# Performance work log

Measured on AMD Instinct MI355X. Metric: run time of the kernel, lower is better.

Reference implementation:

```python
import jax, jax.numpy as jnp
import numpy as np

ALPHA = 0.2

def _ema_last_weights(T, alpha, dtype):
    # Closed form for the final EMA value after the sequential recurrence:
    # ema_T = (1-a)^(T-1) * x_0 + sum_{t=1}^{T-1} a*(1-a)^(T-1-t) * x_t
    t = jnp.arange(T)
    w = alpha * (1.0 - alpha) ** (T - 1 - t)
    w = w.at[0].set((1.0 - alpha) ** (T - 1))
    return w.astype(dtype)


def setup_inputs() -> dict:
    key = jax.random.key(0)
    k1, k2 = jax.random.split(key)
    B, T, F = 64, 2048, 256
    x = jax.random.normal(k1, (B, T, F), dtype=jnp.float32)
    W = jax.random.normal(k2, (F, F), dtype=jnp.float32) * (1.0 / np.sqrt(F))
    b = jnp.zeros((F,), dtype=jnp.float32)
    return {"x": x, "W": W, "b": b}


def reference(x, W, b):
    B, T, F = x.shape
    # final-step EMA over time (equivalent to the sequential python loop)
    w = _ema_last_weights(T, ALPHA, x.dtype)          # [T]
    last_ref = jnp.einsum('t,btf->bf', w, x)[:, None, :]  # [B,1,F]
    # base residual predictor: per-timestep linear
    res = jnp.einsum('btf,fg->btg', x, W) + b          # [B,T,F]
    return last_ref + res
```

## Files before the change

kernel.cpp:

```cpp
#include <hip/hip_runtime.h>
#include <hip/hip_bf16.h>

#define Bdim 64
#define Tdim 2048
#define Fdim 256
#define TAIL 256
#define NCH 8
#define CHT 32

#define BM 64
#define BK 64
#define ASTR 72
#define BSTR 72

typedef __bf16 bf16x8 __attribute__((ext_vector_type(8)));
typedef float f32x16 __attribute__((ext_vector_type(16)));
typedef unsigned short u16x8 __attribute__((ext_vector_type(8)));

__device__ __forceinline__ unsigned short bf16_rne(float f) {
  unsigned int u = __float_as_uint(f);
  u += 0x7FFFu + ((u >> 16) & 1u);
  return (unsigned short)(u >> 16);
}

__global__ void prep_wt(const float* __restrict__ W, unsigned short* __restrict__ Wt) {
  int i = blockIdx.x * 256 + threadIdx.x;
  int g = i >> 8, f = i & 255;
  Wt[i] = bf16_rne(W[f * Fdim + g]);
}

__global__ void ema_partial(const float* __restrict__ x, float* __restrict__ part) {
  int b = blockIdx.x, c = blockIdx.y, f = threadIdx.x;
  int t0 = Tdim - TAIL + c * CHT;
  float w = 0.2f * exp2f((float)(Tdim - 1 - t0) * -0.32192809488736235f);
  const float* xp = x + ((size_t)b * Tdim + t0) * Fdim + f;
  float s = 0.f;
#pragma unroll
  for (int j = 0; j < CHT; ++j) {
    s += w * xp[(size_t)j * Fdim];
    w *= 1.25f;
  }
  part[(c * Bdim + b) * Fdim + f] = s;
}

__global__ __launch_bounds__(256, 3)
void gemm_fused(const float* __restrict__ x, const unsigned short* __restrict__ Wt,
                const float* __restrict__ bias, const float* __restrict__ part,
                float* __restrict__ out) {
  __shared__ unsigned short Abuf[BM * ASTR];
  __shared__ unsigned short Bbuf[Fdim * BSTR];
  __shared__ float lref[Fdim];

  const int tid = threadIdx.x;
  const int blk = blockIdx.x;
  const int b = blk >> 5;
  const size_t row0 = (size_t)blk * BM;

  {
    float s = bias[tid];
#pragma unroll
    for (int c = 0; c < NCH; ++c) s += part[(c * Bdim + b) * Fdim + tid];
    lref[tid] = s;
  }

  const int wave = tid >> 6;
  const int lane = tid & 63;
  const int lm = lane & 31;
  const int half = lane >> 5;

  f32x16 acc[2][2] = {};

  const int g8 = (tid & 7) * 8;
  const int arow = tid >> 3;

  for (int kc = 0; kc < 4; ++kc) {
    const int k0 = kc * BK;
#pragma unroll
    for (int p = 0; p < 2; ++p) {
      int r = arow + p * 32;
      const float* src = &x[(row0 + r) * Fdim + k0 + g8];
      float4 v0 = *(const float4*)src;
      float4 v1 = *(const float4*)(src + 4);
      u16x8 w;
      w[0] = bf16_rne(v0.x); w[1] = bf16_rne(v0.y);
      w[2] = bf16_rne(v0.z); w[3] = bf16_rne(v0.w);
      w[4] = bf16_rne(v1.x); w[5] = bf16_rne(v1.y);
      w[6] = bf16_rne(v1.z); w[7] = bf16_rne(v1.w);
      *(u16x8*)&Abuf[r * ASTR + g8] = w;
    }
#pragma unroll
    for (int p = 0; p < 8; ++p) {
      int n = arow + p * 32;
      u16x8 wv = *(const u16x8*)&Wt[n * Fdim + k0 + g8];
      *(u16x8*)&Bbuf[n * BSTR + g8] = wv;
    }
    __syncthreads();

    const int ko = half * 8;
#pragma unroll
    for (int s = 0; s < 4; ++s) {
      int kk = s * 16 + ko;
      bf16x8 a0 = *(const bf16x8*)&Abuf[(lm) * ASTR + kk];
      bf16x8 a1 = *(const bf16x8*)&Abuf[(32 + lm) * ASTR + kk];
      bf16x8 b0 = *(const bf16x8*)&Bbuf[(wave * 64 + lm) * BSTR + kk];
      bf16x8 b1 = *(const bf16x8*)&Bbuf[(wave * 64 + 32 + lm) * BSTR + kk];
      acc[0][0] = __builtin_amdgcn_mfma_f32_32x32x16_bf16(a0, b0, acc[0][0], 0, 0, 0);
      acc[0][1] = __builtin_amdgcn_mfma_f32_32x32x16_bf16(a0, b1, acc[0][1], 0, 0, 0);
      acc[1][0] = __builtin_amdgcn_mfma_f32_32x32x16_bf16(a1, b0, acc[1][0], 0, 0, 0);
      acc[1][1] = __builtin_amdgcn_mfma_f32_32x32x16_bf16(a1, b1, acc[1][1], 0, 0, 0);
    }
    __syncthreads();
  }

  float* op = out + row0 * Fdim;
  const int rbase = 4 * half;
#pragma unroll
  for (int i = 0; i < 2; ++i) {
#pragma unroll
    for (int j = 0; j < 2; ++j) {
      int n = wave * 64 + j * 32 + lm;
      float lb = lref[n];
#pragma unroll
      for (int r = 0; r < 16; ++r) {
        int rowi = i * 32 + (r & 3) + 8 * (r >> 2) + rbase;
        op[(size_t)rowi * Fdim + n] = acc[i][j][r] + lb;
      }
    }
  }
}

extern "C" void kernel_launch(void* const* d_in, const int* in_sizes, int n_in,
                              void* d_out, int out_size, void* d_ws, size_t ws_size,
                              hipStream_t stream) {
  const float* x = (const float*)d_in[0];
  const float* W = (const float*)d_in[1];
  const float* bias = (const float*)d_in[2];
  float* out = (float*)d_out;

  unsigned short* Wt = (unsigned short*)d_ws;
  float* part = (float*)((char*)d_ws + Fdim * Fdim * sizeof(unsigned short));

  prep_wt<<<Fdim, 256, 0, stream>>>(W, Wt);
  ema_partial<<<dim3(Bdim, NCH), 256, 0, stream>>>(x, part);
  gemm_fused<<<(Bdim * Tdim) / BM, 256, 0, stream>>>(x, Wt, bias, part, out);
}
```

Before: 242.3 us.

## Double-buffer GEMM LDS tiles with register prefetch, XOR swizzle, and merged prep kernels

Restructures the GEMM main loop into 8 chunks of K=32, with double-buffered LDS tiles. Global loads for the next chunks are prefetched into registers while MFMAs run on the current buffer. Padded LDS strides are replaced by an XOR swizzle, and only one barrier per chunk is needed. The W transpose and the EMA partial kernels are merged into one launch to cut a kernel launch. This costs more registers for the prefetch state, which may pressure occupancy at 3 blocks per CU.

```diff
diff --git a/kernel.cpp b/kernel.cpp
--- a/kernel.cpp
+++ b/kernel.cpp
@@ -1,5 +1,4 @@
 #include <hip/hip_runtime.h>
-#include <hip/hip_bf16.h>
 
 #define Bdim 64
 #define Tdim 2048
@@ -9,9 +8,8 @@
 #define CHT 32
 
 #define BM 64
-#define BK 64
-#define ASTR 72
-#define BSTR 72
+#define BK 32
+#define NCHUNK 8
 
 typedef __bf16 bf16x8 __attribute__((ext_vector_type(8)));
 typedef float f32x16 __attribute__((ext_vector_type(16)));
@@ -23,38 +21,47 @@
   return (unsigned short)(u >> 16);
 }
 
-__global__ void prep_wt(const float* __restrict__ W, unsigned short* __restrict__ Wt) {
-  int i = blockIdx.x * 256 + threadIdx.x;
-  int g = i >> 8, f = i & 255;
-  Wt[i] = bf16_rne(W[f * Fdim + g]);
-}
-
-__global__ void ema_partial(const float* __restrict__ x, float* __restrict__ part) {
-  int b = blockIdx.x, c = blockIdx.y, f = threadIdx.x;
-  int t0 = Tdim - TAIL + c * CHT;
-  float w = 0.2f * exp2f((float)(Tdim - 1 - t0) * -0.32192809488736235f);
-  const float* xp = x + ((size_t)b * Tdim + t0) * Fdim + f;
-  float s = 0.f;
+__global__ void prep(const float* __restrict__ x, const float* __restrict__ W,
+                     unsigned short* __restrict__ Wt, float* __restrict__ part) {
+  int blk = blockIdx.x;
+  if (blk < Fdim) {
+    int i = blk * 256 + threadIdx.x;
+    int g = i >> 8, f = i & 255;
+    Wt[i] = bf16_rne(W[f * Fdim + g]);
+  } else {
+    int j = blk - Fdim;
+    int b = j & 63, c = j >> 6;
+    int f = threadIdx.x;
+    int t0 = Tdim - TAIL + c * CHT;
+    float w = 0.2f * exp2f((float)(Tdim - 1 - t0) * -0.32192809488736235f);
+    const float* xp = x + ((size_t)b * Tdim + t0) * Fdim + f;
+    float s = 0.f;
 #pragma unroll
-  for (int j = 0; j < CHT; ++j) {
-    s += w * xp[(size_t)j * Fdim];
-    w *= 1.25f;
+    for (int q = 0; q < CHT; ++q) {
+      s += w * xp[(size_t)q * Fdim];
+      w *= 1.25f;
+    }
+    part[(c * Bdim + b) * Fdim + f] = s;
   }
-  part[(c * Bdim + b) * Fdim + f] = s;
 }
 
 __global__ __launch_bounds__(256, 3)
 void gemm_fused(const float* __restrict__ x, const unsigned short* __restrict__ Wt,
                 const float* __restrict__ bias, const float* __restrict__ part,
                 float* __restrict__ out) {
-  __shared__ unsigned short Abuf[BM * ASTR];
-  __shared__ unsigned short Bbuf[Fdim * BSTR];
+  __shared__ unsigned short Abuf[2][BM * BK];
+  __shared__ unsigned short Bbuf[2][Fdim * BK];
   __shared__ float lref[Fdim];
 
   const int tid = threadIdx.x;
   const int blk = blockIdx.x;
   const int b = blk >> 5;
   const size_t row0 = (size_t)blk * BM;
+
+  const int wave = tid >> 6;
+  const int lane = tid & 63;
+  const int lm = lane & 31;
+  const int half = lane >> 5;
 
   {
     float s = bias[tid];
@@ -63,53 +70,85 @@
     lref[tid] = s;
   }
 
-  const int wave = tid >> 6;
-  const int lane = tid & 63;
-  const int lm = lane & 31;
-  const int half = lane >> 5;
+  const int ar = tid >> 2;
+  const int ag = tid & 3;
+  const int aoff = ar * BK + ((ag ^ (ar & 3)) << 3);
+  const float* asrc = x + (row0 + ar) * Fdim + ag * 8;
+
+  const int bn = tid >> 2;
+  const int bg = tid & 3;
+  const unsigned short* bsrc = Wt + (size_t)bn * Fdim + bg * 8;
+  const int boff = bn * BK + ((bg ^ (bn & 3)) << 3);
 
   f32x16 acc[2][2] = {};
+  float4 Ar[2][2];
+  u16x8 br0, br1, br2, br3;
 
-  const int g8 = (tid & 7) * 8;
-  const int arow = tid >> 3;
+  Ar[0][0] = *(const float4*)(asrc);
+  Ar[0][1] = *(const float4*)(asrc + 4);
+  br0 = *(const u16x8*)(bsrc + 0 * 64 * Fdim);
+  br1 = *(const u16x8*)(bsrc + 1 * 64 * Fdim);
+  br2 = *(const u16x8*)(bsrc + 2 * 64 * Fdim);
+  br3 = *(const u16x8*)(bsrc + 3 * 64 * Fdim);
+  {
+    float4 v0 = Ar[0][0], v1 = Ar[0][1];
+    u16x8 w;
+    w[0] = bf16_rne(v0.x); w[1] = bf16_rne(v0.y);
+    w[2] = bf16_rne(v0.z); w[3] = bf16_rne(v0.w);
+    w[4] = bf16_rne(v1.x); w[5] = bf16_rne(v1.y);
+    w[6] = bf16_rne(v1.z); w[7] = bf16_rne(v1.w);
+    *(u16x8*)&Abuf[0][aoff] = w;
+  }
+  *(u16x8*)&Bbuf[0][boff + 0 * 64 * BK] = br0;
+  *(u16x8*)&Bbuf[0][boff + 1 * 64 * BK] = br1;
+  *(u16x8*)&Bbuf[0][boff + 2 * 64 * BK] = br2;
+  *(u16x8*)&Bbuf[0][boff + 3 * 64 * BK] = br3;
+  Ar[1][0] = *(const float4*)(asrc + BK);
+  Ar[1][1] = *(const float4*)(asrc + BK + 4);
+  __syncthreads();
 
-  for (int kc = 0; kc < 4; ++kc) {
-    const int k0 = kc * BK;
 #pragma unroll
-    for (int p = 0; p < 2; ++p) {
-      int r = arow + p * 32;
-      const float* src = &x[(row0 + r) * Fdim + k0 + g8];
-      float4 v0 = *(const float4*)src;
-      float4 v1 = *(const float4*)(src + 4);
+  for (int c = 0; c < NCHUNK; ++c) {
+    const int cur = c & 1, nxt = cur ^ 1;
+    if (c + 2 < NCHUNK) {
+      const float* s4 = asrc + (c + 2) * BK;
+      Ar[cur][0] = *(const float4*)(s4);
+      Ar[cur][1] = *(const float4*)(s4 + 4);
+    }
+    if (c + 1 < NCHUNK) {
+      const unsigned short* bs = bsrc + (c + 1) * BK;
+      br0 = *(const u16x8*)(bs + 0 * 64 * Fdim);
+      br1 = *(const u16x8*)(bs + 1 * 64 * Fdim);
+      br2 = *(const u16x8*)(bs + 2 * 64 * Fdim);
+      br3 = *(const u16x8*)(bs + 3 * 64 * Fdim);
+    }
+#pragma unroll
+    for (int s = 0; s < 2; ++s) {
+      const int G = 2 * s + half;
+      const int sw = ((G ^ (lm & 3)) << 3);
+      bf16x8 a0 = *(const bf16x8*)&Abuf[cur][lm * BK + sw];
+      bf16x8 a1 = *(const bf16x8*)&Abuf[cur][(32 + lm) * BK + sw];
+      bf16x8 b0 = *(const bf16x8*)&Bbuf[cur][(wave * 64 + lm) * BK + sw];
+      bf16x8 b1 = *(const bf16x8*)&Bbuf[cur][(wave * 64 + 32 + lm) * BK + sw];
+      acc[0][0] = __builtin_amdgcn_mfma_f32_32x32x16_bf16(a0, b0, acc[0][0], 0, 0, 0);
+      acc[0][1] = __builtin_amdgcn_mfma_f32_32x32x16_bf16(a0, b1, acc[0][1], 0, 0, 0);
+      acc[1][0] = __builtin_amdgcn_mfma_f32_32x32x16_bf16(a1, b0, acc[1][0], 0, 0, 0);
+      acc[1][1] = __builtin_amdgcn_mfma_f32_32x32x16_bf16(a1, b1, acc[1][1], 0, 0, 0);
+    }
+    if (c + 1 < NCHUNK) {
+      float4 v0 = Ar[nxt][0], v1 = Ar[nxt][1];
       u16x8 w;
       w[0] = bf16_rne(v0.x); w[1] = bf16_rne(v0.y);
       w[2] = bf16_rne(v0.z); w[3] = bf16_rne(v0.w);
       w[4] = bf16_rne(v1.x); w[5] = bf16_rne(v1.y);
       w[6] = bf16_rne(v1.z); w[7] = bf16_rne(v1.w);
-      *(u16x8*)&Abuf[r * ASTR + g8] = w;
+      *(u16x8*)&Abuf[nxt][aoff] = w;
+      *(u16x8*)&Bbuf[nxt][boff + 0 * 64 * BK] = br0;
+      *(u16x8*)&Bbuf[nxt][boff + 1 * 64 * BK] = br1;
+      *(u16x8*)&Bbuf[nxt][boff + 2 * 64 * BK] = br2;
+      *(u16x8*)&Bbuf[nxt][boff + 3 * 64 * BK] = br3;
+      __syncthreads();
     }
-#pragma unroll
-    for (int p = 0; p < 8; ++p) {
-      int n = arow + p * 32;
-      u16x8 wv = *(const u16x8*)&Wt[n * Fdim + k0 + g8];
-      *(u16x8*)&Bbuf[n * BSTR + g8] = wv;
-    }
-    __syncthreads();
-
-    const int ko = half * 8;
-#pragma unroll
-    for (int s = 0; s < 4; ++s) {
-      int kk = s * 16 + ko;
-      bf16x8 a0 = *(const bf16x8*)&Abuf[(lm) * ASTR + kk];
-      bf16x8 a1 = *(const bf16x8*)&Abuf[(32 + lm) * ASTR + kk];
-      bf16x8 b0 = *(const bf16x8*)&Bbuf[(wave * 64 + lm) * BSTR + kk];
-      bf16x8 b1 = *(const bf16x8*)&Bbuf[(wave * 64 + 32 + lm) * BSTR + kk];
-      acc[0][0] = __builtin_amdgcn_mfma_f32_32x32x16_bf16(a0, b0, acc[0][0], 0, 0, 0);
-      acc[0][1] = __builtin_amdgcn_mfma_f32_32x32x16_bf16(a0, b1, acc[0][1], 0, 0, 0);
-      acc[1][0] = __builtin_amdgcn_mfma_f32_32x32x16_bf16(a1, b0, acc[1][0], 0, 0, 0);
-      acc[1][1] = __builtin_amdgcn_mfma_f32_32x32x16_bf16(a1, b1, acc[1][1], 0, 0, 0);
-    }
-    __syncthreads();
   }
 
   float* op = out + row0 * Fdim;
@@ -140,7 +179,6 @@
   unsigned short* Wt = (unsigned short*)d_ws;
   float* part = (float*)((char*)d_ws + Fdim * Fdim * sizeof(unsigned short));
 
-  prep_wt<<<Fdim, 256, 0, stream>>>(W, Wt);
-  ema_partial<<<dim3(Bdim, NCH), 256, 0, stream>>>(x, part);
+  prep<<<Fdim + Bdim * NCH, 256, 0, stream>>>(x, W, Wt, part);
   gemm_fused<<<(Bdim * Tdim) / BM, 256, 0, stream>>>(x, Wt, bias, part, out);
 }
```

Result: slower. 252.4 us (+4.2%).
